# Performance work log

Hardware: AMD Instinct MI355X
Metric: run time of the kernel (lower is better)

## Reference

```python
import jax, jax.numpy as jnp
import numpy as np

N_POINTS = 4096
DIM = 64
MAX_EDGE_LENGTH = 1e9  # large -> no MST edge is filtered, output has static shape (n-1,)


def _mst_edge_lengths(points):
    """0-dim Rips persistence death values == Euclidean MST edge lengths.

    Equivalent to gudhi RipsComplex(max_dimension=0) + flag_persistence_generators
    followed by torch.norm(input[v0] - input[v1], dim=-1). Returned sorted
    ascending (gudhi's ordering is unspecified; compare as a multiset).
    """
    n = points.shape[0]
    sq = jnp.sum(points * points, axis=1)                      # [n]
    d2 = sq[:, None] + sq[None, :] - 2.0 * (points @ points.T)  # [n,n]
    d2 = jnp.maximum(d2, 0.0)
    # safe positive diagonal so sqrt is smooth there (diagonal never selected)
    idx = jnp.arange(n)
    d2 = d2.at[idx, idx].set(1.0)
    D = jnp.sqrt(d2)                                            # [n,n] distances

    inf = jnp.asarray(jnp.inf, D.dtype)
    in_tree0 = jnp.zeros((n,), dtype=bool).at[0].set(True)
    dist0 = jnp.where(in_tree0, inf, D[0])                      # min dist to tree

    def step(carry, _):
        dist, in_tree = carry
        j = jnp.argmin(dist)            # nearest non-tree vertex
        w = dist[j]                     # MST edge length (a persistence death)
        in_tree = in_tree.at[j].set(True)
        dist = jnp.where(in_tree, inf, jnp.minimum(dist, D[j]))
        return (dist, in_tree), w

    _, lengths = jax.lax.scan(step, (dist0, in_tree0), None, length=n - 1)
    # max_edge_length filter is a no-op for MAX_EDGE_LENGTH=1e9
    return jnp.sort(lengths)


def setup_inputs() -> dict:
    key = jax.random.key(0)
    points = jax.random.normal(key, (N_POINTS, DIM), dtype=jnp.float32)
    return {"input": points}


def reference(input) -> jnp.ndarray:
    return _mst_edge_lengths(input)
```

## Files before the change

### kernel.cpp

```cpp
#include <hip/hip_runtime.h>
#include <hip/hip_bf16.h>


#define NPTS 4096
#define SENT 1e30f
#define KINF 0xFFFFFFFFFFFFFFFFull
#define INV32 0xFFFFFFFFu
#define SCAN_ROWS 2
#define SCAN_BLOCKS (NPTS / SCAN_ROWS)
#define CMAX 512

#define HOOK_NORMAL 0
#define HOOK_FORCE_COMPACT 1

typedef short short8 __attribute__((ext_vector_type(8)));
typedef float f32x4 __attribute__((ext_vector_type(4)));

__device__ __forceinline__ float bfbits2f(unsigned int u16) {
  union { unsigned int u; float f; } c;
  c.u = u16 << 16;
  return c.f;
}

__device__ bool data_is_bf16(const unsigned short* p) {
  bool bf = true;
  for (int i = 0; i < 256; ++i) {
    float f = bfbits2f((unsigned int)p[i]);
    if (!(f > -1e6f && f < 1e6f)) bf = false;
  }
  return bf;
}

__global__ __launch_bounds__(256) void prep_kernel(
    const void* pts_raw, unsigned short* Pb, float* sq, int* comp,
    unsigned short* comp16, int* parent, unsigned long long* cheapest,
    float* edges, unsigned* cnt, unsigned* M) {
  float pf = bfbits2f((unsigned int)((const unsigned short*)pts_raw)[threadIdx.x]);
  const bool bfs = (bool)__syncthreads_and((int)(pf > -1e6f && pf < 1e6f));

  const int g = blockIdx.x * 256 + threadIdx.x;
  if (g < NPTS) {
    comp[g] = g;
    comp16[g] = (unsigned short)g;
    parent[g] = g;
    cheapest[g] = KINF;
  }
  M[g] = INV32;
  if (g == NPTS - 1) edges[NPTS - 1] = SENT;
  if (g == 0) {
    cnt[0] = 0u;
    cnt[1] = 0u;
    cnt[2] = bfs ? 1u : 0u;
    cnt[3] = 0u;
  }

  const int row = g >> 6;
  const int lane = threadIdx.x & 63;

  unsigned short ub;
  if (bfs) {
    ub = ((const unsigned short*)pts_raw)[row * 64 + lane];
  } else {
    __hip_bfloat16 h = __float2bfloat16(((const float*)pts_raw)[row * 64 + lane]);
    ub = *(unsigned short*)&h;
  }
  Pb[row * 64 + lane] = ub;

  float v = bfbits2f((unsigned int)ub);
  float s = v * v;
#pragma unroll
  for (int m = 1; m < 64; m <<= 1) s += __shfl_xor(s, m);
  if (lane == 0) sq[row] = s;
}

__global__ __launch_bounds__(256) void dist_mfma(const unsigned short* Pb,
                                                 const float* sq,
                                                 unsigned short* Dbf,
                                                 unsigned long long* cheapest) {
  __shared__ unsigned short tile[64 * 72];

  const int t = threadIdx.x;
  const int w = t >> 6, lane = t & 63;
  const int quad = lane >> 4, l16 = lane & 15;
  const int rbase = blockIdx.y * 64 + w * 16;
  const int cbase = blockIdx.x * 64;

  const short8* Pv = (const short8*)Pb;
  short8 a0 = Pv[(rbase + l16) * 8 + quad];
  short8 a1 = Pv[(rbase + l16) * 8 + quad + 4];

  f32x4 acc[4];
#pragma unroll
  for (int c = 0; c < 4; ++c) {
    short8 b0 = Pv[(cbase + c * 16 + l16) * 8 + quad];
    short8 b1 = Pv[(cbase + c * 16 + l16) * 8 + quad + 4];
    f32x4 z = {0.f, 0.f, 0.f, 0.f};
    z = __builtin_amdgcn_mfma_f32_16x16x32_bf16(a0, b0, z, 0, 0, 0);
    z = __builtin_amdgcn_mfma_f32_16x16x32_bf16(a1, b1, z, 0, 0, 0);
    acc[c] = z;
  }

  float sr[4];
#pragma unroll
  for (int q = 0; q < 4; ++q) sr[q] = sq[rbase + quad * 4 + q];

#pragma unroll
  for (int c = 0; c < 4; ++c) {
    float sc = sq[cbase + c * 16 + l16];
#pragma unroll
    for (int q = 0; q < 4; ++q) {
      float d2 = sr[q] + sc - 2.f * acc[c][q];
      float dd = sqrtf(fmaxf(d2, 0.f));
      __hip_bfloat16 h = __float2bfloat16(dd);
      tile[(w * 16 + quad * 4 + q) * 72 + c * 16 + l16] = *(unsigned short*)&h;
    }
  }
  __syncthreads();

  for (int i = t; i < 512; i += 256) {
    int row = i >> 3, cb8 = (i & 7) * 8;
    uint4 v = *(const uint4*)&tile[row * 72 + cb8];
    *(uint4*)&Dbf[(size_t)(blockIdx.y * 64 + row) * 4096 + cbase + cb8] = v;
  }

  {
    const int r = t >> 2, cseg = (t & 3) * 16;
    const int v = blockIdx.y * 64 + r;
    const uint4* lrow = (const uint4*)&tile[r * 72 + cseg];
    uint4 v0 = lrow[0], v1 = lrow[1];
    unsigned wv[16] = {v0.x & 0xFFFFu, v0.x >> 16, v0.y & 0xFFFFu, v0.y >> 16,
                       v0.z & 0xFFFFu, v0.z >> 16, v0.w & 0xFFFFu, v0.w >> 16,
                       v1.x & 0xFFFFu, v1.x >> 16, v1.y & 0xFFFFu, v1.y >> 16,
                       v1.z & 0xFFFFu, v1.z >> 16, v1.w & 0xFFFFu, v1.w >> 16};
    unsigned long long kmin = KINF;
#pragma unroll
    for (int e = 0; e < 16; ++e) {
      const int j = cbase + cseg + e;
      if (j != v) {
        unsigned ed = (v < j) ? (((unsigned)v << 12) | (unsigned)j)
                              : (((unsigned)j << 12) | (unsigned)v);
        unsigned long long key = ((unsigned long long)wv[e] << 24) | ed;
        kmin = key < kmin ? key : kmin;
      }
    }
#pragma unroll
    for (int m = 1; m < 4; m <<= 1) {
      unsigned long long o = __shfl_xor(kmin, m);
      kmin = o < kmin ? o : kmin;
    }
    if ((t & 3) == 0) atomicMin(&cheapest[v], kmin);
  }
}

__global__ __launch_bounds__(256) void bor_scan(const unsigned short* Dbf,
                                                const unsigned short* comp16,
                                                int* parent,
                                                unsigned long long* cheapest,
                                                const unsigned* cnt) {
  if (cnt[1]) return;

  __shared__ unsigned long long redu[SCAN_ROWS][4];

  const int t = threadIdx.x;
  const int b = blockIdx.x;
  const int wave = t >> 6;
  const int gtid = b * 256 + t;
  const int vbase = b * SCAN_ROWS;

  if (gtid < NPTS) parent[gtid] = gtid;

  const uint4* c16v = (const uint4*)comp16;
  uint4 c0 = c16v[2 * t], c1 = c16v[2 * t + 1];
  unsigned mc[16] = {c0.x & 0xFFFFu, c0.x >> 16, c0.y & 0xFFFFu, c0.y >> 16,
                     c0.z & 0xFFFFu, c0.z >> 16, c0.w & 0xFFFFu, c0.w >> 16,
                     c1.x & 0xFFFFu, c1.x >> 16, c1.y & 0xFFFFu, c1.y >> 16,
                     c1.z & 0xFFFFu, c1.z >> 16, c1.w & 0xFFFFu, c1.w >> 16};

  const uint4* rp = (const uint4*)(Dbf + (size_t)vbase * NPTS);
#pragma unroll
  for (int vv = 0; vv < SCAN_ROWS; ++vv) {
    const int v = vbase + vv;
    const unsigned cv = (unsigned)comp16[v];
    uint4 a0 = rp[vv * 512 + 2 * t];
    uint4 a1 = rp[vv * 512 + 2 * t + 1];
    unsigned wv[16] = {a0.x & 0xFFFFu, a0.x >> 16, a0.y & 0xFFFFu, a0.y >> 16,
                       a0.z & 0xFFFFu, a0.z >> 16, a0.w & 0xFFFFu, a0.w >> 16,
                       a1.x & 0xFFFFu, a1.x >> 16, a1.y & 0xFFFFu, a1.y >> 16,
                       a1.z & 0xFFFFu, a1.z >> 16, a1.w & 0xFFFFu, a1.w >> 16};
    unsigned long long kmin = KINF;
#pragma unroll
    for (int e = 0; e < 16; ++e) {
      const int j = t * 16 + e;
      if (mc[e] != cv) {
        unsigned ed = (v < j) ? (((unsigned)v << 12) | (unsigned)j)
                              : (((unsigned)j << 12) | (unsigned)v);
        unsigned long long key = ((unsigned long long)wv[e] << 24) | ed;
        kmin = key < kmin ? key : kmin;
      }
    }
#pragma unroll
    for (int m = 1; m < 64; m <<= 1) {
      unsigned long long o = __shfl_xor(kmin, m);
      kmin = o < kmin ? o : kmin;
    }
    if ((t & 63) == 0) redu[vv][wave] = kmin;
  }
  __syncthreads();

  if (t < SCAN_ROWS) {
    unsigned long long k = redu[t][0];
    if (redu[t][1] < k) k = redu[t][1];
    if (redu[t][2] < k) k = redu[t][2];
    if (redu[t][3] < k) k = redu[t][3];
    if (k != KINF) atomicMin(&cheapest[(int)comp16[vbase + t]], k);
  }
}

__global__ __launch_bounds__(1024) void bor_hook(int* comp,
                                                 unsigned short* comp16,
                                                 int* parent,
                                                 unsigned long long* cheapest,
                                                 float* edges, unsigned* cnt,
                                                 int mode) {
  if (cnt[1]) return;
  const int t = threadIdx.x;

  for (int i = t; i < NPTS; i += 1024) {
    if (comp[i] == i) {
      unsigned long long key = cheapest[i];
      if (key != KINF) {
        int mx = (int)(key & 0xFFFull);
        int mn = (int)((key >> 12) & 0xFFFull);
        int ca = comp[mn], cb = comp[mx];
        int u = (ca == i) ? cb : ca;
        bool mutual = (cheapest[u] == key);
        if (!mutual || i < u) {
          unsigned pos = atomicAdd(cnt, 1u);
          edges[pos] = bfbits2f((unsigned)(key >> 24));
        }
        if (!mutual || i > u) parent[i] = u;
      }
    }
  }
  __threadfence_block();
  __syncthreads();

  for (int i = t; i < NPTS; i += 1024) {
    int r = comp[i], p;
    for (int it = 0; it < NPTS; ++it) {
      p = parent[r];
      if (p == r) break;
      r = p;
    }
    comp[i] = r;
    comp16[i] = (unsigned short)r;
    cheapest[i] = KINF;
  }
  __threadfence_block();
  __syncthreads();

  if (mode == HOOK_FORCE_COMPACT) {
    for (int i = t; i < NPTS; i += 1024)
      if (comp[i] == i) parent[i] = (int)atomicAdd(&cnt[3], 1u);
    __syncthreads();
    for (int i = t; i < NPTS; i += 1024)
      comp16[i] = (unsigned short)parent[comp[i]];
  }
  if (t == 0 && cnt[0] >= (unsigned)(NPTS - 1)) cnt[1] = 1u;
}

__global__ __launch_bounds__(256) void bor_project(const unsigned short* Dbf,
                                                   const unsigned short* comp16,
                                                   unsigned* M,
                                                   const unsigned* cnt) {
  if (cnt[1]) return;

  __shared__ unsigned Mloc[SCAN_ROWS][CMAX];
  const int t = threadIdx.x;
  const int b = blockIdx.x;
  const int vbase = b * SCAN_ROWS;

  Mloc[0][t] = INV32;
  Mloc[0][t + 256] = INV32;
  Mloc[1][t] = INV32;
  Mloc[1][t + 256] = INV32;
  __syncthreads();

  const uint4* c16v = (const uint4*)comp16;
  uint4 c0 = c16v[2 * t], c1 = c16v[2 * t + 1];
  unsigned mc[16] = {c0.x & 0xFFFFu, c0.x >> 16, c0.y & 0xFFFFu, c0.y >> 16,
                     c0.z & 0xFFFFu, c0.z >> 16, c0.w & 0xFFFFu, c0.w >> 16,
                     c1.x & 0xFFFFu, c1.x >> 16, c1.y & 0xFFFFu, c1.y >> 16,
                     c1.z & 0xFFFFu, c1.z >> 16, c1.w & 0xFFFFu, c1.w >> 16};

  const uint4* rp = (const uint4*)(Dbf + (size_t)vbase * NPTS);
#pragma unroll
  for (int vv = 0; vv < SCAN_ROWS; ++vv) {
    const unsigned cv = (unsigned)comp16[vbase + vv];
    uint4 a0 = rp[vv * 512 + 2 * t];
    uint4 a1 = rp[vv * 512 + 2 * t + 1];
    unsigned wv[16] = {a0.x & 0xFFFFu, a0.x >> 16, a0.y & 0xFFFFu, a0.y >> 16,
                       a0.z & 0xFFFFu, a0.z >> 16, a0.w & 0xFFFFu, a0.w >> 16,
                       a1.x & 0xFFFFu, a1.x >> 16, a1.y & 0xFFFFu, a1.y >> 16,
                       a1.z & 0xFFFFu, a1.z >> 16, a1.w & 0xFFFFu, a1.w >> 16};
#pragma unroll
    for (int e = 0; e < 16; ++e)
      if (mc[e] != cv) atomicMin(&Mloc[vv][mc[e]], wv[e]);
  }
  __syncthreads();

  const unsigned cv0 = (unsigned)comp16[vbase];
  const unsigned cv1 = (unsigned)comp16[vbase + 1];
#pragma unroll
  for (int s = 0; s < 2; ++s) {
    const int col = t + 256 * s;
    unsigned x = Mloc[0][col];
    if (x != INV32) atomicMin(&M[cv0 * CMAX + col], x);
    unsigned y = Mloc[1][col];
    if (y != INV32) atomicMin(&M[cv1 * CMAX + col], y);
  }
}

__global__ __launch_bounds__(1024) void bor_finish(const unsigned* M,
                                                   unsigned* cnt,
                                                   float* edges) {
  if (cnt[1]) return;

  __shared__ int comp2[CMAX];
  __shared__ int parent2[CMAX];
  __shared__ unsigned long long cheap2[CMAX];
  __shared__ int live;

  const int t = threadIdx.x;
  const int C = (int)cnt[3];
  if (t < CMAX) comp2[t] = t;
  __syncthreads();

  for (int round = 0; round < 10; ++round) {
    if (t < CMAX) cheap2[t] = KINF;
    if (t == 0) live = 0;
    __syncthreads();

    {
      const int c = t >> 1, q = t & 1;
      if (c < C) {
        const int cc = comp2[c];
        unsigned long long kmin = KINF;
        const uint4* Mr = (const uint4*)(M + c * CMAX + q * 256);
#pragma unroll 4
        for (int g = 0; g < 64; ++g) {
          uint4 m4 = Mr[g];
          const int j0 = q * 256 + g * 4;
          unsigned wj[4] = {m4.x, m4.y, m4.z, m4.w};
#pragma unroll
          for (int k = 0; k < 4; ++k) {
            int j = j0 + k;
            unsigned w = wj[k];
            if (w != INV32 && comp2[j] != cc) {
              int lo = c < j ? c : j, hi = c < j ? j : c;
              unsigned long long key = ((unsigned long long)w << 20) |
                                       ((unsigned)lo << 10) | (unsigned)hi;
              if (key < kmin) kmin = key;
            }
          }
        }
        if (kmin != KINF) atomicMin(&cheap2[cc], kmin);
      }
    }
    __syncthreads();

    if (t < CMAX) {
      parent2[t] = t;
      if (comp2[t] == t) {
        unsigned long long key = cheap2[t];
        if (key != KINF) {
          int hi = (int)(key & 0x3FFull);
          int lo = (int)((key >> 10) & 0x3FFull);
          int ca = comp2[lo], cb = comp2[hi];
          int u = (ca == t) ? cb : ca;
          bool mutual = (cheap2[u] == key);
          if (!mutual || t < u) {
            unsigned pos = atomicAdd(cnt, 1u);
            edges[pos] = bfbits2f((unsigned)(key >> 20));
          }
          if (!mutual || t > u) parent2[t] = u;
        }
      }
    }
    __syncthreads();

    if (t < CMAX) {
      int r = comp2[t], p;
      for (int it = 0; it < CMAX; ++it) {
        p = parent2[r];
        if (p == r) break;
        r = p;
      }
      comp2[t] = r;
      if (t < C && r != comp2[0]) live = 1;
    }
    __syncthreads();
    if (!live) break;
  }
}

__global__ __launch_bounds__(256) void rank_sort(const float* edges,
                                                 const unsigned* cnt,
                                                 void* out) {
  __shared__ unsigned long long wred[4][2];
  const int b = blockIdx.x;
  const int t = threadIdx.x;
  const int pbase = 4 * b;
  const float4* ev = (const float4*)edges;
  const float4 pvv = ev[b];
  const float pv0 = pvv.x, pv1 = pvv.y, pv2 = pvv.z, pv3 = pvv.w;

  int c0 = 0, c1 = 0, c2 = 0, c3 = 0;
#pragma unroll
  for (int k = 0; k < 4; ++k) {
    float4 e = ev[t + 256 * k];
    int j = 4 * (t + 256 * k);
    float va[4] = {e.x, e.y, e.z, e.w};
#pragma unroll
    for (int m = 0; m < 4; ++m) {
      const float x = va[m];
      const int xi = j + m;
      c0 += (x < pv0 || (x == pv0 && xi < pbase + 0));
      c1 += (x < pv1 || (x == pv1 && xi < pbase + 1));
      c2 += (x < pv2 || (x == pv2 && xi < pbase + 2));
      c3 += (x < pv3 || (x == pv3 && xi < pbase + 3));
    }
  }

  unsigned long long p0 = (unsigned long long)(unsigned)c0 |
                          ((unsigned long long)(unsigned)c1 << 32);
  unsigned long long p1 = (unsigned long long)(unsigned)c2 |
                          ((unsigned long long)(unsigned)c3 << 32);
#pragma unroll
  for (int m = 1; m < 64; m <<= 1) {
    p0 += __shfl_xor(p0, m);
    p1 += __shfl_xor(p1, m);
  }
  if ((t & 63) == 0) { wred[t >> 6][0] = p0; wred[t >> 6][1] = p1; }
  __syncthreads();

  if (t == 0) {
    unsigned long long a = wred[0][0] + wred[1][0] + wred[2][0] + wred[3][0];
    unsigned long long d = wred[0][1] + wred[1][1] + wred[2][1] + wred[3][1];
    const int r[4] = {(int)(a & 0xFFFFFFFFull), (int)(a >> 32),
                      (int)(d & 0xFFFFFFFFull), (int)(d >> 32)};
    const float pv[4] = {pv0, pv1, pv2, pv3};
    const bool bf = cnt[2] != 0u;
#pragma unroll
    for (int p = 0; p < 4; ++p) {
      const int pidx = pbase + p;
      if (pidx < NPTS - 1) {
        if (bf) ((__hip_bfloat16*)out)[r[p]] = __float2bfloat16(pv[p]);
        else    ((float*)out)[r[p]] = pv[p];
      }
    }
  }
}

__global__ __launch_bounds__(256) void dist_kernel(const void* pts_raw,
                                                   __hip_bfloat16* Dbf) {
  __shared__ float As[64 * 65];
  __shared__ float Bs[64 * 65];
  __shared__ float sqA[64];
  __shared__ float sqB[64];

  const int t = threadIdx.x;
  const int bx = blockIdx.x, by = blockIdx.y;
  const bool bf = data_is_bf16((const unsigned short*)pts_raw);
  const unsigned short* pu = (const unsigned short*)pts_raw;
  const float* pf = (const float*)pts_raw;

  for (int s = 0; s < 16; ++s) {
    int e = t + 256 * s;
    int r = e >> 6, c = e & 63;
    float av, bv;
    if (bf) {
      av = bfbits2f((unsigned int)pu[by * 4096 + e]);
      bv = bfbits2f((unsigned int)pu[bx * 4096 + e]);
    } else {
      av = pf[by * 4096 + e];
      bv = pf[bx * 4096 + e];
    }
    As[r * 65 + c] = av;
    Bs[r * 65 + c] = bv;
  }
  __syncthreads();

  if (t < 64) {
    float s = 0.f;
    for (int k = 0; k < 64; ++k) { float x = As[t * 65 + k]; s += x * x; }
    sqA[t] = s;
  } else if (t < 128) {
    int r = t - 64;
    float s = 0.f;
    for (int k = 0; k < 64; ++k) { float x = Bs[r * 65 + k]; s += x * x; }
    sqB[r] = s;
  }
  __syncthreads();

  const int tx = t & 15, ty = t >> 4;
  const int lr = ty * 4, lc = tx * 4;
  float acc[4][4] = {};
  for (int k = 0; k < 64; ++k) {
    float a[4], b[4];
#pragma unroll
    for (int q = 0; q < 4; ++q) a[q] = As[(lr + q) * 65 + k];
#pragma unroll
    for (int p = 0; p < 4; ++p) b[p] = Bs[(lc + p) * 65 + k];
#pragma unroll
    for (int q = 0; q < 4; ++q)
#pragma unroll
      for (int p = 0; p < 4; ++p) acc[q][p] += a[q] * b[p];
  }

#pragma unroll
  for (int q = 0; q < 4; ++q) {
    int gr = by * 64 + lr + q;
    float sa = sqA[lr + q];
#pragma unroll
    for (int p = 0; p < 4; ++p) {
      int gc = bx * 64 + lc + p;
      float d2 = sa + sqB[lc + p] - 2.f * acc[q][p];
      d2 = fmaxf(d2, 0.f);
      Dbf[(size_t)gr * 4096 + gc] = __float2bfloat16(sqrtf(d2));
    }
  }
}

__global__ __launch_bounds__(512) void prim_kernel(const unsigned short* probe,
                                                   const unsigned short* Dbf,
                                                   void* out) {
  __shared__ float len[NPTS];
  __shared__ float rv[2][8];
  __shared__ int ri[2][8];

  const int t = threadIdx.x;
  const bool bf_out = data_is_bf16(probe);

  float d[8];
  {
    const uint4* row0 = (const uint4*)(Dbf);
    uint4 v = row0[t];
    d[0] = bfbits2f(v.x & 0xffffu); d[1] = bfbits2f(v.x >> 16);
    d[2] = bfbits2f(v.y & 0xffffu); d[3] = bfbits2f(v.y >> 16);
    d[4] = bfbits2f(v.z & 0xffffu); d[5] = bfbits2f(v.z >> 16);
    d[6] = bfbits2f(v.w & 0xffffu); d[7] = bfbits2f(v.w >> 16);
    if (t == 0) d[0] = SENT;
  }

  float bv = SENT;
  int bi = 8 * t;
#pragma unroll
  for (int k = 0; k < 8; ++k)
    if (d[k] < bv) { bv = d[k]; bi = 8 * t + k; }

  for (int step = 0; step < NPTS - 1; ++step) {
    float v = bv;
    int idx = bi;
#pragma unroll
    for (int m = 1; m < 64; m <<= 1) {
      float ov = __shfl_xor(v, m);
      int oi = __shfl_xor(idx, m);
      if (ov < v) { v = ov; idx = oi; }
    }
    const int buf = step & 1;
    if ((t & 63) == 0) { rv[buf][t >> 6] = v; ri[buf][t >> 6] = idx; }
    __syncthreads();

    float w = rv[buf][0];
    int j = ri[buf][0];
#pragma unroll
    for (int u = 1; u < 8; ++u) {
      float uv = rv[buf][u];
      if (uv < w) { w = uv; j = ri[buf][u]; }
    }
    if (t == 0) len[step] = w;

    const uint4* row = (const uint4*)(Dbf + (size_t)j * NPTS);
    uint4 rw = row[t];
    float nd[8];
    nd[0] = bfbits2f(rw.x & 0xffffu); nd[1] = bfbits2f(rw.x >> 16);
    nd[2] = bfbits2f(rw.y & 0xffffu); nd[3] = bfbits2f(rw.y >> 16);
    nd[4] = bfbits2f(rw.z & 0xffffu); nd[5] = bfbits2f(rw.z >> 16);
    nd[6] = bfbits2f(rw.w & 0xffffu); nd[7] = bfbits2f(rw.w >> 16);

    bv = SENT;
    bi = 8 * t;
    const int base = 8 * t;
#pragma unroll
    for (int k = 0; k < 8; ++k) {
      float cur = d[k];
      float nn = fminf(cur, nd[k]);
      if (cur == SENT || base + k == j) nn = SENT;
      d[k] = nn;
      if (nn < bv) { bv = nn; bi = base + k; }
    }
  }

  if (t == 0) len[NPTS - 1] = SENT;
  __syncthreads();

  for (int k = 2; k <= NPTS; k <<= 1) {
    for (int jj = k >> 1; jj > 0; jj >>= 1) {
      for (int i = t; i < NPTS; i += 512) {
        int ixj = i ^ jj;
        if (ixj > i) {
          float a = len[i], b = len[ixj];
          bool up = ((i & k) == 0);
          if ((a > b) == up) { len[i] = b; len[ixj] = a; }
        }
      }
      __syncthreads();
    }
  }

  if (bf_out) {
    __hip_bfloat16* o = (__hip_bfloat16*)out;
    for (int i = t; i < NPTS - 1; i += 512) o[i] = __float2bfloat16(len[i]);
  } else {
    float* o = (float*)out;
    for (int i = t; i < NPTS - 1; i += 512) o[i] = len[i];
  }
}

extern "C" void kernel_launch(void* const* d_in, const int* in_sizes, int n_in,
                              void* d_out, int out_size, void* d_ws, size_t ws_size,
                              hipStream_t stream) {
  const void* pts = d_in[0];
  char* base = (char*)d_ws;
  __hip_bfloat16* Dbf = (__hip_bfloat16*)base;

  size_t off = 32ull << 20;
  int* comp = (int*)(base + off);                  off += (size_t)NPTS * 4;
  int* parent = (int*)(base + off);                off += (size_t)NPTS * 4;
  unsigned long long* cheapest =
      (unsigned long long*)(base + off);           off += (size_t)NPTS * 8;
  float* edges = (float*)(base + off);             off += (size_t)NPTS * 4;
  unsigned* cnt = (unsigned*)(base + off);         off += 256;
  unsigned short* Pb = (unsigned short*)(base + off); off += (size_t)NPTS * 64 * 2;
  float* sq = (float*)(base + off);                off += (size_t)NPTS * 4;
  unsigned short* comp16 = (unsigned short*)(base + off); off += (size_t)NPTS * 2;
  unsigned* M = (unsigned*)(base + off);           off += (size_t)CMAX * CMAX * 4;

  if (ws_size >= off) {
    prep_kernel<<<1024, 256, 0, stream>>>(pts, Pb, sq, comp, comp16, parent,
                                          cheapest, edges, cnt, M);
    const unsigned short* Dus = (const unsigned short*)Dbf;
    dist_mfma<<<dim3(64, 64), 256, 0, stream>>>(Pb, sq, (unsigned short*)Dbf,
                                                cheapest);
    bor_hook<<<1, 1024, 0, stream>>>(comp, comp16, parent, cheapest, edges,
                                     cnt, HOOK_NORMAL);
    bor_scan<<<SCAN_BLOCKS, 256, 0, stream>>>(Dus, comp16, parent, cheapest,
                                              cnt);
    bor_hook<<<1, 1024, 0, stream>>>(comp, comp16, parent, cheapest, edges,
                                     cnt, HOOK_NORMAL);
    bor_scan<<<SCAN_BLOCKS, 256, 0, stream>>>(Dus, comp16, parent, cheapest,
                                              cnt);
    bor_hook<<<1, 1024, 0, stream>>>(comp, comp16, parent, cheapest, edges,
                                     cnt, HOOK_FORCE_COMPACT);
    bor_project<<<SCAN_BLOCKS, 256, 0, stream>>>(Dus, comp16, M, cnt);
    bor_finish<<<1, 1024, 0, stream>>>(M, cnt, edges);
    rank_sort<<<NPTS / 4, 256, 0, stream>>>(edges, cnt, d_out);
  } else {
    dist_kernel<<<dim3(64, 64), 256, 0, stream>>>(pts, Dbf);
    prim_kernel<<<1, 512, 0, stream>>>((const unsigned short*)pts,
                                       (const unsigned short*)Dbf, d_out);
  }
}
```

Baseline: 203.7 us.

## Drop one Boruvka scan round and project to a larger component matrix

Removes one hook+full distance-matrix scan pass and instead compacts components after fewer rounds, raising the component cap to 1024. The projection matrix grows to 1024x1024 and bor_finish now handles up to 1024 components per thread-block, with a wider key packing. This trades one full read of the bf16 distance matrix for larger per-block shared arrays, more atomics in projection and a heavier single-block finish. If more than 1024 components remain after the earlier rounds, the result would be wrong.

Result: faster. 189.7 us (-6.9%).

```diff
diff --git a/kernel.cpp b/kernel.cpp
--- a/kernel.cpp
+++ b/kernel.cpp
@@ -8,7 +8,7 @@
 #define INV32 0xFFFFFFFFu
 #define SCAN_ROWS 2
 #define SCAN_BLOCKS (NPTS / SCAN_ROWS)
-#define CMAX 512
+#define CMAX 1024
 
 #define HOOK_NORMAL 0
 #define HOOK_FORCE_COMPACT 1
@@ -45,7 +45,10 @@
     parent[g] = g;
     cheapest[g] = KINF;
   }
-  M[g] = INV32;
+  {
+    uint4 mi; mi.x = INV32; mi.y = INV32; mi.z = INV32; mi.w = INV32;
+    ((uint4*)M)[g] = mi;
+  }
   if (g == NPTS - 1) edges[NPTS - 1] = SENT;
   if (g == 0) {
     cnt[0] = 0u;
@@ -280,10 +283,11 @@
   const int b = blockIdx.x;
   const int vbase = b * SCAN_ROWS;
 
-  Mloc[0][t] = INV32;
-  Mloc[0][t + 256] = INV32;
-  Mloc[1][t] = INV32;
-  Mloc[1][t + 256] = INV32;
+#pragma unroll
+  for (int s = 0; s < 4; ++s) {
+    Mloc[0][t + 256 * s] = INV32;
+    Mloc[1][t + 256 * s] = INV32;
+  }
   __syncthreads();
 
   const uint4* c16v = (const uint4*)comp16;
@@ -312,7 +316,7 @@
   const unsigned cv0 = (unsigned)comp16[vbase];
   const unsigned cv1 = (unsigned)comp16[vbase + 1];
 #pragma unroll
-  for (int s = 0; s < 2; ++s) {
+  for (int s = 0; s < 4; ++s) {
     const int col = t + 256 * s;
     unsigned x = Mloc[0][col];
     if (x != INV32) atomicMin(&M[cv0 * CMAX + col], x);
@@ -333,24 +337,24 @@
 
   const int t = threadIdx.x;
   const int C = (int)cnt[3];
-  if (t < CMAX) comp2[t] = t;
-  __syncthreads();
-
-  for (int round = 0; round < 10; ++round) {
-    if (t < CMAX) cheap2[t] = KINF;
+  comp2[t] = t;
+  __syncthreads();
+
+  for (int round = 0; round < 11; ++round) {
+    cheap2[t] = KINF;
     if (t == 0) live = 0;
     __syncthreads();
 
     {
-      const int c = t >> 1, q = t & 1;
-      if (c < C) {
+      const int q = t & 1;
+      for (int c = t >> 1; c < C; c += 512) {
         const int cc = comp2[c];
         unsigned long long kmin = KINF;
-        const uint4* Mr = (const uint4*)(M + c * CMAX + q * 256);
+        const uint4* Mr = (const uint4*)(M + c * CMAX + q * 512);
 #pragma unroll 4
-        for (int g = 0; g < 64; ++g) {
+        for (int g = 0; g < 128; ++g) {
           uint4 m4 = Mr[g];
-          const int j0 = q * 256 + g * 4;
+          const int j0 = q * 512 + g * 4;
           unsigned wj[4] = {m4.x, m4.y, m4.z, m4.w};
 #pragma unroll
           for (int k = 0; k < 4; ++k) {
@@ -358,8 +362,8 @@
             unsigned w = wj[k];
             if (w != INV32 && comp2[j] != cc) {
               int lo = c < j ? c : j, hi = c < j ? j : c;
-              unsigned long long key = ((unsigned long long)w << 20) |
-                                       ((unsigned)lo << 10) | (unsigned)hi;
+              unsigned long long key = ((unsigned long long)w << 22) |
+                                       ((unsigned)lo << 11) | (unsigned)hi;
               if (key < kmin) kmin = key;
             }
           }
@@ -369,19 +373,19 @@
     }
     __syncthreads();
 
-    if (t < CMAX) {
+    {
       parent2[t] = t;
       if (comp2[t] == t) {
         unsigned long long key = cheap2[t];
         if (key != KINF) {
-          int hi = (int)(key & 0x3FFull);
-          int lo = (int)((key >> 10) & 0x3FFull);
+          int hi = (int)(key & 0x7FFull);
+          int lo = (int)((key >> 11) & 0x7FFull);
           int ca = comp2[lo], cb = comp2[hi];
           int u = (ca == t) ? cb : ca;
           bool mutual = (cheap2[u] == key);
           if (!mutual || t < u) {
             unsigned pos = atomicAdd(cnt, 1u);
-            edges[pos] = bfbits2f((unsigned)(key >> 20));
+            edges[pos] = bfbits2f((unsigned)(key >> 22));
           }
           if (!mutual || t > u) parent2[t] = u;
         }
@@ -389,7 +393,7 @@
     }
     __syncthreads();
 
-    if (t < CMAX) {
+    {
       int r = comp2[t], p;
       for (int it = 0; it < CMAX; ++it) {
         p = parent2[r];
@@ -653,10 +657,6 @@
     const unsigned short* Dus = (const unsigned short*)Dbf;
     dist_mfma<<<dim3(64, 64), 256, 0, stream>>>(Pb, sq, (unsigned short*)Dbf,
                                                 cheapest);
-    bor_hook<<<1, 1024, 0, stream>>>(comp, comp16, parent, cheapest, edges,
-                                     cnt, HOOK_NORMAL);
-    bor_scan<<<SCAN_BLOCKS, 256, 0, stream>>>(Dus, comp16, parent, cheapest,
-                                              cnt);
     bor_hook<<<1, 1024, 0, stream>>>(comp, comp16, parent, cheapest, edges,
                                      cnt, HOOK_NORMAL);
     bor_scan<<<SCAN_BLOCKS, 256, 0, stream>>>(Dus, comp16, parent, cheapest,
```
